# Kernel optimization log

Hardware: AMD Instinct MI355X
Metric: run time of the kernel (lower is better)

## Reference

```python
import jax, jax.numpy as jnp
import numpy as np

EPS = 1e-5
DIM_HEAD = 64
HEADS = 16
SCALE = DIM_HEAD ** -0.5


def rotate_half(x):
    # '... (j d) -> ... j d' with j=2, then (-x2, x1)
    x = x.reshape(*x.shape[:-1], 2, x.shape[-1] // 2)
    x1, x2 = x[..., 0, :], x[..., 1, :]
    return jnp.concatenate((-x2, x1), axis=-1)


def apply_rotary(freqs, t):
    # freqs: (n, rot_dim) broadcasts against t: (b, h, n, d)
    rot_dim = freqs.shape[-1]
    t_rot, t_pass = t[..., :rot_dim], t[..., rot_dim:]
    t_rot = t_rot * jnp.cos(freqs) + rotate_half(t_rot) * jnp.sin(freqs)
    return jnp.concatenate((t_rot, t_pass), axis=-1)


def setup_inputs() -> dict:
    key = jax.random.key(0)
    ks = jax.random.split(key, 4)
    b, n, dim = 2, 2048, 1024
    inner = HEADS * DIM_HEAD
    x = jax.random.normal(ks[0], (b, n, dim), dtype=jnp.float32)
    mask = jnp.ones((b, n), dtype=bool)
    rotary_pos_emb = jax.random.normal(ks[1], (n, 32), dtype=jnp.float32)
    W_qkv = jax.random.normal(ks[2], (dim, inner * 3), dtype=jnp.float32) * (dim ** -0.5)
    W_out = jax.random.normal(ks[3], (inner, dim), dtype=jnp.float32) * (inner ** -0.5)
    gamma = jnp.ones((dim,), dtype=jnp.float32)
    return {"x": x, "mask": mask, "rotary_pos_emb": rotary_pos_emb,
            "W_qkv": W_qkv, "W_out": W_out, "gamma": gamma}


def reference(x, mask, rotary_pos_emb, W_qkv, W_out, gamma):
    b, n, _ = x.shape
    qkv = x @ W_qkv  # (b, n, 3*inner)
    q, k, v = jnp.split(qkv, 3, axis=-1)
    def split_heads(t):
        return t.reshape(b, n, HEADS, DIM_HEAD).transpose(0, 2, 1, 3)  # b h n d
    q, k, v = map(split_heads, (q, k, v))
    q = q * SCALE
    q = apply_rotary(rotary_pos_emb, q)
    k = apply_rotary(rotary_pos_emb, k)
    v = apply_rotary(rotary_pos_emb, v)
    sim = jnp.einsum('bhid,bhjd->bhij', q, k)
    mask_value = -jnp.finfo(sim.dtype).max
    sim = jnp.where(mask[:, None, None, :], sim, mask_value)
    sim = sim - jax.lax.stop_gradient(jnp.max(sim, axis=-1, keepdims=True))
    attn = jax.nn.softmax(sim, axis=-1)
    out = jnp.einsum('bhij,bhjd->bhid', attn, v)
    out = out.transpose(0, 2, 1, 3).reshape(b, n, HEADS * DIM_HEAD)
    out = out @ W_out
    # LayerNorm with learned gamma, zero beta
    mean = jnp.mean(out, axis=-1, keepdims=True)
    var = jnp.var(out, axis=-1, keepdims=True)
    out = (out - mean) * jax.lax.rsqrt(var + EPS) * gamma
    return out
```

## Files before the change

### kernel.cpp

```cpp
#include <hip/hip_runtime.h>

typedef __attribute__((ext_vector_type(8))) short s16x8;
typedef __attribute__((ext_vector_type(4))) float f32x4;

#define AS1q __attribute__((address_space(1)))
#define AS3q __attribute__((address_space(3)))

__device__ __forceinline__ void gload16(const void* g, void* l) {
  __builtin_amdgcn_global_load_lds((const AS1q unsigned int*)g,
                                   (AS3q unsigned int*)l, 16, 0, 0);
}

__device__ __forceinline__ unsigned short f2bf(float f) {
  unsigned int u = __float_as_uint(f);
  u = (u + 0x7FFFu + ((u >> 16) & 1u)) >> 16;
  return (unsigned short)u;
}

__device__ __forceinline__ unsigned int cvtpk(float a, float b) {
  unsigned int r;
  asm("v_cvt_pk_bf16_f32 %0, %1, %2" : "=v"(r) : "v"(a), "v"(b));
  return r;
}

__global__ void trig_kernel(const float* __restrict__ rope,
                            float* __restrict__ cosT, float* __restrict__ sinT) {
  int i = blockIdx.x * 256 + threadIdx.x;
  float f = rope[i];
  cosT[i] = cosf(f);
  sinT[i] = sinf(f);
}

__global__ void cast_kernel(const float* __restrict__ in, unsigned short* __restrict__ out) {
  int i = (blockIdx.x * 256 + threadIdx.x) * 4;
  float4 v = *(const float4*)(in + i);
  ushort4 o;
  o.x = f2bf(v.x); o.y = f2bf(v.y); o.z = f2bf(v.z); o.w = f2bf(v.w);
  *(ushort4*)(out + i) = o;
}

__global__ __launch_bounds__(256) void tcast_kernel(const float* __restrict__ in,
    unsigned short* __restrict__ out, int K, int N) {
  __shared__ float tile[32][33];
  int k0 = blockIdx.x * 32, n0 = blockIdx.y * 32;
  int tx = threadIdx.x & 31, ty = threadIdx.x >> 5;
  #pragma unroll
  for (int r = ty; r < 32; r += 8) tile[r][tx] = in[(size_t)(k0 + r) * N + n0 + tx];
  __syncthreads();
  #pragma unroll
  for (int r = ty; r < 32; r += 8) out[(size_t)(n0 + r) * K + k0 + tx] = f2bf(tile[tx][r]);
}

__global__ __launch_bounds__(256) void gemm_bt(
    const unsigned short* __restrict__ A, const unsigned short* __restrict__ Bt,
    float* __restrict__ C, int M, int N, int K, int nbn, int chunk) {
  __shared__ alignas(16) unsigned short Al[2][128 * 64];
  __shared__ alignas(16) unsigned short Bl[2][128 * 64];
  int tid = threadIdx.x, w = tid >> 6, l = tid & 63;
  int l16 = l & 15, lg = l >> 4;
  int lin = (blockIdx.x & 7) * chunk + (blockIdx.x >> 3);
  int m0 = (lin / nbn) * 128, n0 = (lin % nbn) * 128;
  f32x4 acc[4][4] = {};
  int srow0 = w * 8 + (l >> 3);
  int sblk = l & 7;
  auto STAGE = [&](int buf, int k0) {
    #pragma unroll
    for (int c = 0; c < 4; c++) {
      int row = c * 32 + srow0;
      gload16((const char*)A + ((size_t)(m0 + row) * K + k0) * 2 + ((sblk ^ (row & 7)) * 16),
              (char*)Al[buf] + c * 4096 + w * 1024);
      gload16((const char*)Bt + ((size_t)(n0 + row) * K + k0) * 2 + ((sblk ^ (row & 7)) * 16),
              (char*)Bl[buf] + c * 4096 + w * 1024);
    }
  };
  STAGE(0, 0);
  __syncthreads();
  int cur = 0;
  for (int k0 = 0; k0 < K; k0 += 64) {
    if (k0 + 64 < K) STAGE(cur ^ 1, k0 + 64);
    const char* Ac = (const char*)Al[cur];
    const char* Bc = (const char*)Bl[cur];
    #pragma unroll
    for (int kk = 0; kk < 2; kk++) {
      s16x8 af[4], bf[4];
      #pragma unroll
      for (int i = 0; i < 4; i++) {
        int ar = (w >> 1) * 64 + i * 16 + l16;
        int ab = ar * 128 + (kk * 32 + 8 * lg) * 2; ab ^= (ar & 7) << 4;
        af[i] = *(const s16x8*)(Ac + ab);
        int br = (w & 1) * 64 + i * 16 + l16;
        int bb = br * 128 + (kk * 32 + 8 * lg) * 2; bb ^= (br & 7) << 4;
        bf[i] = *(const s16x8*)(Bc + bb);
      }
      #pragma unroll
      for (int i = 0; i < 4; i++)
        #pragma unroll
        for (int j = 0; j < 4; j++)
          acc[i][j] = __builtin_amdgcn_mfma_f32_16x16x32_bf16(af[i], bf[j], acc[i][j], 0, 0, 0);
    }
    __syncthreads();
    cur ^= 1;
  }
  #pragma unroll
  for (int i = 0; i < 4; i++)
    #pragma unroll
    for (int j = 0; j < 4; j++)
      #pragma unroll
      for (int r = 0; r < 4; r++) {
        int mrow = m0 + (w >> 1) * 64 + i * 16 + 4 * lg + r;
        int ncol = n0 + (w & 1) * 64 + j * 16 + l16;
        C[(size_t)mrow * N + ncol] = acc[i][j][r];
      }
}

__global__ __launch_bounds__(256) void gemm_qkv(
    const unsigned short* __restrict__ A, const unsigned short* __restrict__ Bt,
    const float* __restrict__ cosT, const float* __restrict__ sinT,
    unsigned short* __restrict__ Qb, unsigned short* __restrict__ Kb,
    unsigned short* __restrict__ Vb, int K) {
  __shared__ alignas(16) char smem[65536];
  float (*cs)[68] = (float(*)[68])smem;
  int tid = threadIdx.x, w = tid >> 6, l = tid & 63;
  int l16 = l & 15, lg = l >> 4;
  int lin = (blockIdx.x & 7) * 96 + (blockIdx.x >> 3);
  int m0 = (lin / 24) * 128, n0 = (lin % 24) * 128;
  f32x4 acc[4][4] = {};
  int srow0 = w * 8 + (l >> 3);
  int sblk = l & 7;
  auto STAGE = [&](int buf, int k0) {
    char* Ad = smem + buf * 16384;
    char* Bd = smem + 32768 + buf * 16384;
    #pragma unroll
    for (int c = 0; c < 4; c++) {
      int row = c * 32 + srow0;
      gload16((const char*)A + ((size_t)(m0 + row) * K + k0) * 2 + ((sblk ^ (row & 7)) * 16),
              Ad + c * 4096 + w * 1024);
      gload16((const char*)Bt + ((size_t)(n0 + row) * K + k0) * 2 + ((sblk ^ (row & 7)) * 16),
              Bd + c * 4096 + w * 1024);
    }
  };
  STAGE(0, 0);
  __syncthreads();
  int cur = 0;
  for (int k0 = 0; k0 < K; k0 += 64) {
    if (k0 + 64 < K) STAGE(cur ^ 1, k0 + 64);
    const char* Ac = smem + cur * 16384;
    const char* Bc = smem + 32768 + cur * 16384;
    #pragma unroll
    for (int kk = 0; kk < 2; kk++) {
      s16x8 af[4], bf[4];
      #pragma unroll
      for (int i = 0; i < 4; i++) {
        int ar = (w >> 1) * 64 + i * 16 + l16;
        int ab = ar * 128 + (kk * 32 + 8 * lg) * 2; ab ^= (ar & 7) << 4;
        af[i] = *(const s16x8*)(Ac + ab);
        int br = (w & 1) * 64 + i * 16 + l16;
        int bb = br * 128 + (kk * 32 + 8 * lg) * 2; bb ^= (br & 7) << 4;
        bf[i] = *(const s16x8*)(Bc + bb);
      }
      #pragma unroll
      for (int i = 0; i < 4; i++)
        #pragma unroll
        for (int j = 0; j < 4; j++)
          acc[i][j] = __builtin_amdgcn_mfma_f32_16x16x32_bf16(af[i], bf[j], acc[i][j], 0, 0, 0);
    }
    __syncthreads();
    cur ^= 1;
  }
  int b = m0 >> 11;
  int nnb = m0 & 2047;
  for (int g = tid; g < 128 * 16; g += 256) {
    int row = g >> 4;
    int c4 = (g & 15) * 4;
    float4 val;
    if (c4 < 32) val = *(const float4*)(cosT + (size_t)(nnb + row) * 32 + c4);
    else         val = *(const float4*)(sinT + (size_t)(nnb + row) * 32 + (c4 - 32));
    *(float4*)&cs[row][c4] = val;
  }
  __syncthreads();
  int section = n0 >> 10;
  int h = ((n0 & 1023) >> 6) + (w & 1);
  unsigned short* dst = section == 0 ? Qb : (section == 1 ? Kb : Vb);
  float scl = section == 0 ? 0.18033688011112042f : 1.0f;
  #pragma unroll
  for (int i = 0; i < 4; i++)
    #pragma unroll
    for (int r = 0; r < 4; r++) {
      int lrow = (w >> 1) * 64 + i * 16 + 4 * lg + r;
      float c0 = cs[lrow][l16],      s0 = cs[lrow][32 + l16];
      float c1 = cs[lrow][16 + l16], s1 = cs[lrow][48 + l16];
      float a0 = acc[i][0][r], a1 = acc[i][1][r];
      float o0 = (c0 * a0 - s0 * a1) * scl;
      float o1 = (c1 * a1 + s1 * a0) * scl;
      float o2 = acc[i][2][r] * scl;
      float o3 = acc[i][3][r] * scl;
      int nn = nnb + lrow;
      size_t obase = ((size_t)(b * 16 + h) * 2048 + nn) * 64;
      dst[obase + l16]      = f2bf(o0);
      dst[obase + 16 + l16] = f2bf(o1);
      dst[obase + 32 + l16] = f2bf(o2);
      dst[obase + 48 + l16] = f2bf(o3);
    }
}

__global__ __launch_bounds__(256) void vtrans_kernel(const unsigned short* __restrict__ Vb,
                                                     unsigned short* __restrict__ Vt) {
  __shared__ unsigned short vt[64][65];
  int nb = blockIdx.x, bh = blockIdx.y;
  int t = threadIdx.x;
  int nl = t >> 2, quarter = t & 3;
  size_t src = ((size_t)bh * 2048 + nb * 64 + nl) * 64 + quarter * 16;
  s16x8 v0 = *(const s16x8*)(Vb + src);
  s16x8 v1 = *(const s16x8*)(Vb + src + 8);
  #pragma unroll
  for (int i = 0; i < 8; i++) {
    vt[nl][quarter * 16 + i] = (unsigned short)v0[i];
    vt[nl][quarter * 16 + 8 + i] = (unsigned short)v1[i];
  }
  __syncthreads();
  int drow = t >> 2;
  size_t dstb = ((size_t)bh * 64 + drow) * 2048 + (size_t)nb * 64 + (size_t)quarter * 16;
  s16x8 o0, o1;
  #pragma unroll
  for (int j = 0; j < 8; j++) {
    int p = quarter * 16 + j;
    int c = 32 * (p >> 5) + 16 * ((p >> 2) & 1) + 4 * ((p >> 3) & 3) + (p & 3);
    o0[j] = (short)vt[c][drow];
  }
  #pragma unroll
  for (int j = 0; j < 8; j++) {
    int p = quarter * 16 + 8 + j;
    int c = 32 * (p >> 5) + 16 * ((p >> 2) & 1) + 4 * ((p >> 3) & 3) + (p & 3);
    o1[j] = (short)vt[c][drow];
  }
  *(s16x8*)(Vt + dstb) = o0;
  *(s16x8*)(Vt + dstb + 8) = o1;
}

__global__ __launch_bounds__(256) void flash_kernel(
    const unsigned short* __restrict__ Q, const unsigned short* __restrict__ K,
    const unsigned short* __restrict__ Vt, unsigned short* __restrict__ A2) {
  __shared__ alignas(16) unsigned short Kl[2][128 * 64];
  __shared__ alignas(16) unsigned short Vl[2][2][64 * 64];
  int id = blockIdx.x;
  int s = id >> 3;
  int bh = (id & 7) * 4 + (s >> 4);
  int qblk = s & 15;
  int tid = threadIdx.x, w = tid >> 6, l = tid & 63;
  int l16 = l & 15, lg = l >> 4;
  size_t base = (size_t)bh * 2048 * 64;
  const unsigned short* Qb = Q + base;
  const unsigned short* Kb = K + base;
  const unsigned short* Vb = Vt + base;
  int q0 = qblk * 128 + w * 16;
  s16x8 qfA[2], qfB[2];
  {
    const s16x8* qpA = (const s16x8*)(Qb + (size_t)(q0 + l16) * 64);
    qfA[0] = qpA[lg]; qfA[1] = qpA[lg + 4];
    const s16x8* qpB = (const s16x8*)(Qb + (size_t)(q0 + 64 + l16) * 64);
    qfB[0] = qpB[lg]; qfB[1] = qpB[lg + 4];
  }
  s16x8 ones;
  #pragma unroll
  for (int i = 0; i < 8; i++) ones[i] = (short)0x3F80;
  f32x4 oA[4], oB[4], o5A, o5B;
  {
    f32x4 z = {0.f, 0.f, 0.f, 0.f};
    #pragma unroll
    for (int nd = 0; nd < 4; nd++) { oA[nd] = z; oB[nd] = z; }
    o5A = z; o5B = z;
  }
  int srow0 = w * 8 + (l >> 3);
  int sblk = l & 7;
  auto STAGE = [&](int buf, int t0) {
    #pragma unroll
    for (int c = 0; c < 4; c++) {
      int row = c * 32 + srow0;
      gload16((const char*)Kb + (size_t)(t0 + row) * 128 + ((sblk ^ (row & 7)) * 16),
              (char*)Kl[buf] + c * 4096 + w * 1024);
    }
    #pragma unroll
    for (int s2 = 0; s2 < 2; s2++)
      #pragma unroll
      for (int c = 0; c < 2; c++) {
        int row = c * 32 + srow0;
        gload16((const char*)Vb + (size_t)row * 4096 + (size_t)(t0 + s2 * 64) * 2 + ((sblk ^ (row & 7)) * 16),
                (char*)Vl[buf][s2] + c * 4096 + w * 1024);
      }
  };
  STAGE(0, 0);
  __syncthreads();
  int cur = 0;
  for (int t0 = 0; t0 < 2048; t0 += 128) {
    if (t0 + 128 < 2048) STAGE(cur ^ 1, t0 + 128);
    #pragma unroll
    for (int sub = 0; sub < 2; sub++) {
      const char* Kc = (const char*)Kl[cur] + sub * 8192;
      const char* Vc = (const char*)Vl[cur][sub];
      f32x4 sfA[4], sfB[4];
      __builtin_amdgcn_s_setprio(1);
      #pragma unroll
      for (int nbt = 0; nbt < 4; nbt++) {
        f32x4 z = {0.f, 0.f, 0.f, 0.f};
        sfA[nbt] = z; sfB[nbt] = z;
        #pragma unroll
        for (int kk = 0; kk < 2; kk++) {
          int kvrow = nbt * 16 + l16;
          int byte_ = kvrow * 128 + (kk * 32 + 8 * lg) * 2;
          byte_ ^= (kvrow & 7) << 4;
          s16x8 bfr = *(const s16x8*)(Kc + byte_);
          sfA[nbt] = __builtin_amdgcn_mfma_f32_16x16x32_bf16(bfr, qfA[kk], sfA[nbt], 0, 0, 0);
          sfB[nbt] = __builtin_amdgcn_mfma_f32_16x16x32_bf16(bfr, qfB[kk], sfB[nbt], 0, 0, 0);
        }
      }
      __builtin_amdgcn_s_setprio(0);
      s16x8 paA0, paA1, paB0, paB1;
      {
        float e0[4], e1[4], e2[4], e3[4];
        #pragma unroll
        for (int r = 0; r < 4; r++) {
          e0[r] = __builtin_amdgcn_exp2f(sfA[0][r]);
          e1[r] = __builtin_amdgcn_exp2f(sfA[1][r]);
          e2[r] = __builtin_amdgcn_exp2f(sfA[2][r]);
          e3[r] = __builtin_amdgcn_exp2f(sfA[3][r]);
        }
        unsigned int* w0 = (unsigned int*)&paA0;
        unsigned int* w1 = (unsigned int*)&paA1;
        w0[0] = cvtpk(e0[0], e0[1]); w0[1] = cvtpk(e0[2], e0[3]);
        w0[2] = cvtpk(e1[0], e1[1]); w0[3] = cvtpk(e1[2], e1[3]);
        w1[0] = cvtpk(e2[0], e2[1]); w1[1] = cvtpk(e2[2], e2[3]);
        w1[2] = cvtpk(e3[0], e3[1]); w1[3] = cvtpk(e3[2], e3[3]);
      }
      {
        float e0[4], e1[4], e2[4], e3[4];
        #pragma unroll
        for (int r = 0; r < 4; r++) {
          e0[r] = __builtin_amdgcn_exp2f(sfB[0][r]);
          e1[r] = __builtin_amdgcn_exp2f(sfB[1][r]);
          e2[r] = __builtin_amdgcn_exp2f(sfB[2][r]);
          e3[r] = __builtin_amdgcn_exp2f(sfB[3][r]);
        }
        unsigned int* w0 = (unsigned int*)&paB0;
        unsigned int* w1 = (unsigned int*)&paB1;
        w0[0] = cvtpk(e0[0], e0[1]); w0[1] = cvtpk(e0[2], e0[3]);
        w0[2] = cvtpk(e1[0], e1[1]); w0[3] = cvtpk(e1[2], e1[3]);
        w1[0] = cvtpk(e2[0], e2[1]); w1[1] = cvtpk(e2[2], e2[3]);
        w1[2] = cvtpk(e3[0], e3[1]); w1[3] = cvtpk(e3[2], e3[3]);
      }
      __builtin_amdgcn_s_setprio(1);
      #pragma unroll
      for (int nk = 0; nk < 2; nk++) {
        s16x8 pA = nk ? paA1 : paA0;
        s16x8 pB = nk ? paB1 : paB0;
        #pragma unroll
        for (int nd = 0; nd < 4; nd++) {
          int drow = nd * 16 + l16;
          int vb = drow * 128 + (nk * 32 + 8 * lg) * 2;
          vb ^= (drow & 7) << 4;
          s16x8 vfr = *(const s16x8*)(Vc + vb);
          oA[nd] = __builtin_amdgcn_mfma_f32_16x16x32_bf16(pA, vfr, oA[nd], 0, 0, 0);
          oB[nd] = __builtin_amdgcn_mfma_f32_16x16x32_bf16(pB, vfr, oB[nd], 0, 0, 0);
        }
        o5A = __builtin_amdgcn_mfma_f32_16x16x32_bf16(pA, ones, o5A, 0, 0, 0);
        o5B = __builtin_amdgcn_mfma_f32_16x16x32_bf16(pB, ones, o5B, 0, 0, 0);
      }
      __builtin_amdgcn_s_setprio(0);
    }
    __syncthreads();
    cur ^= 1;
  }
  float rsA[4], rsB[4];
  #pragma unroll
  for (int r = 0; r < 4; r++) {
    rsA[r] = __builtin_amdgcn_rcpf(o5A[r]);
    rsB[r] = __builtin_amdgcn_rcpf(o5B[r]);
  }
  int b = bh >> 4, h = bh & 15;
  #pragma unroll
  for (int nd = 0; nd < 4; nd++)
    #pragma unroll
    for (int r = 0; r < 4; r++) {
      int qA = q0 + 4 * lg + r;
      int d = nd * 16 + l16;
      A2[((size_t)(b * 2048 + qA)) * 1024 + h * 64 + d] = f2bf(oA[nd][r] * rsA[r]);
      A2[((size_t)(b * 2048 + qA + 64)) * 1024 + h * 64 + d] = f2bf(oB[nd][r] * rsB[r]);
    }
}

__global__ __launch_bounds__(256) void ln_kernel(const float* __restrict__ in,
    const float* __restrict__ gamma, float* __restrict__ out) {
  __shared__ float red[8];
  int row = blockIdx.x, t = threadIdx.x;
  const float* r = in + (size_t)row * 1024;
  float4 v = *(const float4*)(r + t * 4);
  float s = v.x + v.y + v.z + v.w;
  float s2 = v.x * v.x + v.y * v.y + v.z * v.z + v.w * v.w;
  #pragma unroll
  for (int off = 1; off < 64; off <<= 1) { s += __shfl_xor(s, off); s2 += __shfl_xor(s2, off); }
  if ((t & 63) == 0) { red[t >> 6] = s; red[4 + (t >> 6)] = s2; }
  __syncthreads();
  float S = red[0] + red[1] + red[2] + red[3];
  float S2 = red[4] + red[5] + red[6] + red[7];
  float mean = S * (1.f / 1024.f);
  float var = S2 * (1.f / 1024.f) - mean * mean;
  float inv = rsqrtf(var + 1e-5f);
  float4 g = *(const float4*)(gamma + t * 4);
  float4 ov;
  ov.x = (v.x - mean) * inv * g.x;
  ov.y = (v.y - mean) * inv * g.y;
  ov.z = (v.z - mean) * inv * g.z;
  ov.w = (v.w - mean) * inv * g.w;
  *(float4*)(out + (size_t)row * 1024 + t * 4) = ov;
}

extern "C" void kernel_launch(void* const* d_in, const int* in_sizes, int n_in,
                              void* d_out, int out_size, void* d_ws, size_t ws_size,
                              hipStream_t stream) {
  const float* x     = (const float*)d_in[0];
  const float* rope  = (const float*)d_in[2];
  const float* Wqkv  = (const float*)d_in[3];
  const float* Wout  = (const float*)d_in[4];
  const float* gamma = (const float*)d_in[5];
  float* out = (float*)d_out;

  char* ws = (char*)d_ws;
  unsigned short* Qb  = (unsigned short*)(ws + 0);
  unsigned short* Kb  = (unsigned short*)(ws + 8388608);
  unsigned short* Vb  = (unsigned short*)(ws + 16777216);
  unsigned short* Vt  = (unsigned short*)(ws + 25165824);
  float*          out2= (float*)(ws + 33554432);
  unsigned short* xb  = (unsigned short*)(ws + 50331648);
  unsigned short* wqT = (unsigned short*)(ws + 58720256);
  unsigned short* woT = (unsigned short*)(ws + 65011712);
  float*          cosT= (float*)(ws + 67108864);
  float*          sinT= (float*)(ws + 67371008);
  unsigned short* a2 = xb;

  trig_kernel<<<256, 256, 0, stream>>>(rope, cosT, sinT);
  cast_kernel<<<4096, 256, 0, stream>>>(x, xb);
  tcast_kernel<<<dim3(32, 96), 256, 0, stream>>>(Wqkv, wqT, 1024, 3072);
  tcast_kernel<<<dim3(32, 32), 256, 0, stream>>>(Wout, woT, 1024, 1024);
  gemm_qkv<<<768, 256, 0, stream>>>(xb, wqT, cosT, sinT, Qb, Kb, Vb, 1024);
  vtrans_kernel<<<dim3(32, 32), 256, 0, stream>>>(Vb, Vt);
  flash_kernel<<<512, 256, 0, stream>>>(Qb, Kb, Vt, a2);
  gemm_bt<<<256, 256, 0, stream>>>(a2, woT, out2, 4096, 1024, 1024, 8, 32);
  ln_kernel<<<4096, 256, 0, stream>>>(out2, gamma, out);
}
```

Baseline: 129.3 us.

## Switch flash attention to triple-buffered 64-key stages with vmcnt-based waits

Replaces the double-buffered 128-key K/V staging with a three-slot ring of 64-key tiles, keeping two tiles in flight. Each iteration waits only on the older tile with s_waitcnt vmcnt(4) plus a raw barrier, rather than a full __syncthreads after each 128-key block. The loop body moves into a lambda, and LDS use drops from 64KB to 48KB per block, which may allow more resident blocks. In exchange there is one barrier per 64 keys instead of per 128, and correctness relies on the hand-counted outstanding loads.

```diff
diff --git a/kernel.cpp b/kernel.cpp
--- a/kernel.cpp
+++ b/kernel.cpp
@@ -240,8 +240,8 @@
 __global__ __launch_bounds__(256) void flash_kernel(
     const unsigned short* __restrict__ Q, const unsigned short* __restrict__ K,
     const unsigned short* __restrict__ Vt, unsigned short* __restrict__ A2) {
-  __shared__ alignas(16) unsigned short Kl[2][128 * 64];
-  __shared__ alignas(16) unsigned short Vl[2][2][64 * 64];
+  __shared__ alignas(16) unsigned short Kl[3][64 * 64];
+  __shared__ alignas(16) unsigned short Vl[3][64 * 64];
   int id = blockIdx.x;
   int s = id >> 3;
   int bh = (id & 7) * 4 + (s >> 4);
@@ -274,101 +274,104 @@
   int sblk = l & 7;
   auto STAGE = [&](int buf, int t0) {
     #pragma unroll
-    for (int c = 0; c < 4; c++) {
+    for (int c = 0; c < 2; c++) {
       int row = c * 32 + srow0;
       gload16((const char*)Kb + (size_t)(t0 + row) * 128 + ((sblk ^ (row & 7)) * 16),
               (char*)Kl[buf] + c * 4096 + w * 1024);
-    }
-    #pragma unroll
-    for (int s2 = 0; s2 < 2; s2++)
-      #pragma unroll
-      for (int c = 0; c < 2; c++) {
-        int row = c * 32 + srow0;
-        gload16((const char*)Vb + (size_t)row * 4096 + (size_t)(t0 + s2 * 64) * 2 + ((sblk ^ (row & 7)) * 16),
-                (char*)Vl[buf][s2] + c * 4096 + w * 1024);
-      }
+      gload16((const char*)Vb + (size_t)row * 4096 + (size_t)t0 * 2 + ((sblk ^ (row & 7)) * 16),
+              (char*)Vl[buf] + c * 4096 + w * 1024);
+    }
+  };
+  auto BODY = [&](int cb) {
+    const char* Kc = (const char*)Kl[cb];
+    const char* Vc = (const char*)Vl[cb];
+    f32x4 sfA[4], sfB[4];
+    __builtin_amdgcn_s_setprio(1);
+    #pragma unroll
+    for (int nbt = 0; nbt < 4; nbt++) {
+      f32x4 z = {0.f, 0.f, 0.f, 0.f};
+      sfA[nbt] = z; sfB[nbt] = z;
+      #pragma unroll
+      for (int kk = 0; kk < 2; kk++) {
+        int kvrow = nbt * 16 + l16;
+        int byte_ = kvrow * 128 + (kk * 32 + 8 * lg) * 2;
+        byte_ ^= (kvrow & 7) << 4;
+        s16x8 bfr = *(const s16x8*)(Kc + byte_);
+        sfA[nbt] = __builtin_amdgcn_mfma_f32_16x16x32_bf16(bfr, qfA[kk], sfA[nbt], 0, 0, 0);
+        sfB[nbt] = __builtin_amdgcn_mfma_f32_16x16x32_bf16(bfr, qfB[kk], sfB[nbt], 0, 0, 0);
+      }
+    }
+    __builtin_amdgcn_s_setprio(0);
+    s16x8 paA0, paA1, paB0, paB1;
+    {
+      float e0[4], e1[4], e2[4], e3[4];
+      #pragma unroll
+      for (int r = 0; r < 4; r++) {
+        e0[r] = __builtin_amdgcn_exp2f(sfA[0][r]);
+        e1[r] = __builtin_amdgcn_exp2f(sfA[1][r]);
+        e2[r] = __builtin_amdgcn_exp2f(sfA[2][r]);
+        e3[r] = __builtin_amdgcn_exp2f(sfA[3][r]);
+      }
+      unsigned int* w0 = (unsigned int*)&paA0;
+      unsigned int* w1 = (unsigned int*)&paA1;
+      w0[0] = cvtpk(e0[0], e0[1]); w0[1] = cvtpk(e0[2], e0[3]);
+      w0[2] = cvtpk(e1[0], e1[1]); w0[3] = cvtpk(e1[2], e1[3]);
+      w1[0] = cvtpk(e2[0], e2[1]); w1[1] = cvtpk(e2[2], e2[3]);
+      w1[2] = cvtpk(e3[0], e3[1]); w1[3] = cvtpk(e3[2], e3[3]);
+    }
+    {
+      float e0[4], e1[4], e2[4], e3[4];
+      #pragma unroll
+      for (int r = 0; r < 4; r++) {
+        e0[r] = __builtin_amdgcn_exp2f(sfB[0][r]);
+        e1[r] = __builtin_amdgcn_exp2f(sfB[1][r]);
+        e2[r] = __builtin_amdgcn_exp2f(sfB[2][r]);
+        e3[r] = __builtin_amdgcn_exp2f(sfB[3][r]);
+      }
+      unsigned int* w0 = (unsigned int*)&paB0;
+      unsigned int* w1 = (unsigned int*)&paB1;
+      w0[0] = cvtpk(e0[0], e0[1]); w0[1] = cvtpk(e0[2], e0[3]);
+      w0[2] = cvtpk(e1[0], e1[1]); w0[3] = cvtpk(e1[2], e1[3]);
+      w1[0] = cvtpk(e2[0], e2[1]); w1[1] = cvtpk(e2[2], e2[3]);
+      w1[2] = cvtpk(e3[0], e3[1]); w1[3] = cvtpk(e3[2], e3[3]);
+    }
+    __builtin_amdgcn_s_setprio(1);
+    #pragma unroll
+    for (int nk = 0; nk < 2; nk++) {
+      s16x8 pA = nk ? paA1 : paA0;
+      s16x8 pB = nk ? paB1 : paB0;
+      #pragma unroll
+      for (int nd = 0; nd < 4; nd++) {
+        int drow = nd * 16 + l16;
+        int vb = drow * 128 + (nk * 32 + 8 * lg) * 2;
+        vb ^= (drow & 7) << 4;
+        s16x8 vfr = *(const s16x8*)(Vc + vb);
+        oA[nd] = __builtin_amdgcn_mfma_f32_16x16x32_bf16(pA, vfr, oA[nd], 0, 0, 0);
+        oB[nd] = __builtin_amdgcn_mfma_f32_16x16x32_bf16(pB, vfr, oB[nd], 0, 0, 0);
+      }
+      o5A = __builtin_amdgcn_mfma_f32_16x16x32_bf16(pA, ones, o5A, 0, 0, 0);
+      o5B = __builtin_amdgcn_mfma_f32_16x16x32_bf16(pB, ones, o5B, 0, 0, 0);
+    }
+    __builtin_amdgcn_s_setprio(0);
   };
   STAGE(0, 0);
-  __syncthreads();
+  STAGE(1, 64);
   int cur = 0;
-  for (int t0 = 0; t0 < 2048; t0 += 128) {
-    if (t0 + 128 < 2048) STAGE(cur ^ 1, t0 + 128);
-    #pragma unroll
-    for (int sub = 0; sub < 2; sub++) {
-      const char* Kc = (const char*)Kl[cur] + sub * 8192;
-      const char* Vc = (const char*)Vl[cur][sub];
-      f32x4 sfA[4], sfB[4];
-      __builtin_amdgcn_s_setprio(1);
-      #pragma unroll
-      for (int nbt = 0; nbt < 4; nbt++) {
-        f32x4 z = {0.f, 0.f, 0.f, 0.f};
-        sfA[nbt] = z; sfB[nbt] = z;
-        #pragma unroll
-        for (int kk = 0; kk < 2; kk++) {
-          int kvrow = nbt * 16 + l16;
-          int byte_ = kvrow * 128 + (kk * 32 + 8 * lg) * 2;
-          byte_ ^= (kvrow & 7) << 4;
-          s16x8 bfr = *(const s16x8*)(Kc + byte_);
-          sfA[nbt] = __builtin_amdgcn_mfma_f32_16x16x32_bf16(bfr, qfA[kk], sfA[nbt], 0, 0, 0);
-          sfB[nbt] = __builtin_amdgcn_mfma_f32_16x16x32_bf16(bfr, qfB[kk], sfB[nbt], 0, 0, 0);
-        }
-      }
-      __builtin_amdgcn_s_setprio(0);
-      s16x8 paA0, paA1, paB0, paB1;
-      {
-        float e0[4], e1[4], e2[4], e3[4];
-        #pragma unroll
-        for (int r = 0; r < 4; r++) {
-          e0[r] = __builtin_amdgcn_exp2f(sfA[0][r]);
-          e1[r] = __builtin_amdgcn_exp2f(sfA[1][r]);
-          e2[r] = __builtin_amdgcn_exp2f(sfA[2][r]);
-          e3[r] = __builtin_amdgcn_exp2f(sfA[3][r]);
-        }
-        unsigned int* w0 = (unsigned int*)&paA0;
-        unsigned int* w1 = (unsigned int*)&paA1;
-        w0[0] = cvtpk(e0[0], e0[1]); w0[1] = cvtpk(e0[2], e0[3]);
-        w0[2] = cvtpk(e1[0], e1[1]); w0[3] = cvtpk(e1[2], e1[3]);
-        w1[0] = cvtpk(e2[0], e2[1]); w1[1] = cvtpk(e2[2], e2[3]);
-        w1[2] = cvtpk(e3[0], e3[1]); w1[3] = cvtpk(e3[2], e3[3]);
-      }
-      {
-        float e0[4], e1[4], e2[4], e3[4];
-        #pragma unroll
-        for (int r = 0; r < 4; r++) {
-          e0[r] = __builtin_amdgcn_exp2f(sfB[0][r]);
-          e1[r] = __builtin_amdgcn_exp2f(sfB[1][r]);
-          e2[r] = __builtin_amdgcn_exp2f(sfB[2][r]);
-          e3[r] = __builtin_amdgcn_exp2f(sfB[3][r]);
-        }
-        unsigned int* w0 = (unsigned int*)&paB0;
-        unsigned int* w1 = (unsigned int*)&paB1;
-        w0[0] = cvtpk(e0[0], e0[1]); w0[1] = cvtpk(e0[2], e0[3]);
-        w0[2] = cvtpk(e1[0], e1[1]); w0[3] = cvtpk(e1[2], e1[3]);
-        w1[0] = cvtpk(e2[0], e2[1]); w1[1] = cvtpk(e2[2], e2[3]);
-        w1[2] = cvtpk(e3[0], e3[1]); w1[3] = cvtpk(e3[2], e3[3]);
-      }
-      __builtin_amdgcn_s_setprio(1);
-      #pragma unroll
-      for (int nk = 0; nk < 2; nk++) {
-        s16x8 pA = nk ? paA1 : paA0;
-        s16x8 pB = nk ? paB1 : paB0;
-        #pragma unroll
-        for (int nd = 0; nd < 4; nd++) {
-          int drow = nd * 16 + l16;
-          int vb = drow * 128 + (nk * 32 + 8 * lg) * 2;
-          vb ^= (drow & 7) << 4;
-          s16x8 vfr = *(const s16x8*)(Vc + vb);
-          oA[nd] = __builtin_amdgcn_mfma_f32_16x16x32_bf16(pA, vfr, oA[nd], 0, 0, 0);
-          oB[nd] = __builtin_amdgcn_mfma_f32_16x16x32_bf16(pB, vfr, oB[nd], 0, 0, 0);
-        }
-        o5A = __builtin_amdgcn_mfma_f32_16x16x32_bf16(pA, ones, o5A, 0, 0, 0);
-        o5B = __builtin_amdgcn_mfma_f32_16x16x32_bf16(pB, ones, o5B, 0, 0, 0);
-      }
-      __builtin_amdgcn_s_setprio(0);
-    }
-    __syncthreads();
-    cur ^= 1;
-  }
+  for (int i = 0; i < 31; i++) {
+    asm volatile("s_waitcnt vmcnt(4)" ::: "memory");
+    __builtin_amdgcn_s_barrier();
+    __builtin_amdgcn_sched_barrier(0);
+    if (i < 30) {
+      int nb = cur + 2; if (nb >= 3) nb -= 3;
+      STAGE(nb, (i + 2) * 64);
+    }
+    BODY(cur);
+    cur++; if (cur >= 3) cur -= 3;
+  }
+  asm volatile("s_waitcnt vmcnt(0)" ::: "memory");
+  __builtin_amdgcn_s_barrier();
+  __builtin_amdgcn_sched_barrier(0);
+  BODY(cur);
   float rsA[4], rsB[4];
   #pragma unroll
   for (int r = 0; r < 4; r++) {
```

Measured after the change: 136.1 us. 1.05x slower.
